# Optimization experiments

Measured on AMD Instinct MI355X. Metric: run time of the kernel, lower is better.

Reference implementation:

```python
import jax, jax.numpy as jnp
import numpy as np

NUM_VIRUSES = 50000
NUM_DRUGS = 50000
EMBED_DIM = 128
NUM_LAYERS = 3
NUM_INTERACTIONS = 800000  # undirected virus-drug pairs -> 1.6M directed edges


def setup_inputs() -> dict:
    key = jax.random.key(0)
    k1, k2, k3, k4 = jax.random.split(key, 4)
    n_nodes = NUM_VIRUSES + NUM_DRUGS
    # random bipartite interactions (virus -> global drug index)
    v = jax.random.randint(k1, (NUM_INTERACTIONS,), 0, NUM_VIRUSES)
    d = jax.random.randint(k2, (NUM_INTERACTIONS,), 0, NUM_DRUGS) + NUM_VIRUSES
    # symmetric adjacency: both directions
    edge_row = jnp.concatenate([v, d]).astype(jnp.int32)
    edge_col = jnp.concatenate([d, v]).astype(jnp.int32)
    # symmetric normalization D^{-1/2} A D^{-1/2}
    deg = jnp.zeros((n_nodes,), jnp.float32).at[edge_row].add(1.0)
    dinv_sqrt = jnp.where(deg > 0, jax.lax.rsqrt(jnp.maximum(deg, 1.0)), 0.0)
    edge_val = dinv_sqrt[edge_row] * dinv_sqrt[edge_col]
    virus_emb = jax.random.normal(k3, (NUM_VIRUSES, EMBED_DIM), dtype=jnp.float32) * 0.1
    drug_emb = jax.random.normal(k4, (NUM_DRUGS, EMBED_DIM), dtype=jnp.float32) * 0.1
    return {
        "edge_row": edge_row,
        "edge_col": edge_col,
        "edge_val": edge_val,
        "virus_emb": virus_emb,
        "drug_emb": drug_emb,
    }


def reference(edge_row, edge_col, edge_val, virus_emb, drug_emb):
    num_viruses = virus_emb.shape[0]
    n_nodes = num_viruses + drug_emb.shape[0]
    # initial layer-0 embeddings
    x = jnp.concatenate([virus_emb, drug_emb], axis=0)  # [N, D]
    acc = x  # running sum over layers (fused mean)
    h = x
    for _ in range(NUM_LAYERS):
        # SpMM: h <- A_norm @ h  via gather + segment_sum over COO edges
        msgs = edge_val[:, None] * h[edge_col]            # [nnz, D]
        h = jax.ops.segment_sum(msgs, edge_row, num_segments=n_nodes)
        acc = acc + h
    final = acc / jnp.asarray(NUM_LAYERS + 1, acc.dtype)  # mean over L+1 layers
    return final[:num_viruses, :], final[num_viruses:, :]
```

## Files before the change

### kernel.cpp

```cpp
#include <hip/hip_runtime.h>
#include <hip/hip_fp16.h>

static constexpr int D = 128;
static constexpr int RPB_LOG = 10;
static constexpr int RPB = 1 << RPB_LOG;
static constexpr int MAX_BINS = 1024;
static constexpr int CHUNK = 8192;

__global__ void binCount(const int* __restrict__ erow, int* __restrict__ bin_cnt,
                         int E, int nbins) {
    __shared__ int hist[MAX_BINS];
    int t = threadIdx.x;
    int e0 = blockIdx.x * CHUNK;
    for (int i = t; i < nbins; i += 256) hist[i] = 0;
    __syncthreads();
    for (int k = 0; k < CHUNK / 256; ++k) {
        int e = e0 + t + k * 256;
        if (e < E) atomicAdd(&hist[erow[e] >> RPB_LOG], 1);
    }
    __syncthreads();
    for (int b = t; b < nbins; b += 256)
        if (hist[b]) atomicAdd(&bin_cnt[b], hist[b]);
}

__global__ void scanBins(const int* __restrict__ bin_cnt, int* __restrict__ bin_base,
                         int* __restrict__ gcur, int nbins, int E) {
    __shared__ int sm[MAX_BINS];
    int t = threadIdx.x;
    int v = (t < nbins) ? bin_cnt[t] : 0;
    sm[t] = v;
    __syncthreads();
    for (int off = 1; off < MAX_BINS; off <<= 1) {
        int x = sm[t];
        int y = (t >= off) ? sm[t - off] : 0;
        __syncthreads();
        sm[t] = x + y;
        __syncthreads();
    }
    if (t < nbins) {
        int excl = sm[t] - v;
        bin_base[t] = excl;
        gcur[t] = excl;
    }
    if (t == 0) bin_base[nbins] = E;
}

__global__ void binA(const int* __restrict__ erow, const int* __restrict__ ecol,
                     int* __restrict__ gcur, int2* __restrict__ tmp, int E, int nbins) {
    __shared__ int hist[MAX_BINS];
    __shared__ int base[MAX_BINS];
    __shared__ int lcur[MAX_BINS];
    int t = threadIdx.x;
    int e0 = blockIdx.x * CHUNK;
    for (int i = t; i < nbins; i += 256) { hist[i] = 0; lcur[i] = 0; }
    __syncthreads();
    for (int k = 0; k < CHUNK / 256; ++k) {
        int e = e0 + t + k * 256;
        if (e < E) atomicAdd(&hist[erow[e] >> RPB_LOG], 1);
    }
    __syncthreads();
    for (int b = t; b < nbins; b += 256)
        base[b] = hist[b] ? atomicAdd(&gcur[b], hist[b]) : 0;
    __syncthreads();
    for (int k = 0; k < CHUNK / 256; ++k) {
        int e = e0 + t + k * 256;
        if (e < E) {
            int r = erow[e];
            int b = r >> RPB_LOG;
            int pos = base[b] + atomicAdd(&lcur[b], 1);
            tmp[pos] = make_int2(r, ecol[e]);
        }
    }
}

__global__ void binB(const int2* __restrict__ tmp, const int* __restrict__ bin_base,
                     int* __restrict__ row_ptr, float* __restrict__ dinv,
                     float* __restrict__ rdinv, int* __restrict__ col_s,
                     int N, int E, int nbins) {
    __shared__ int cnt[RPB];
    __shared__ int sm[RPB];
    __shared__ int cur[RPB];
    int b = blockIdx.x;
    int r0 = b << RPB_LOG;
    int t = threadIdx.x;
    cnt[t] = 0;
    __syncthreads();
    int start = bin_base[b];
    int end = bin_base[b + 1];
    for (int p = start + t; p < end; p += RPB)
        atomicAdd(&cnt[tmp[p].x - r0], 1);
    __syncthreads();
    int v = cnt[t];
    sm[t] = v;
    __syncthreads();
    for (int off = 1; off < RPB; off <<= 1) {
        int x = sm[t];
        int y = (t >= off) ? sm[t - off] : 0;
        __syncthreads();
        sm[t] = x + y;
        __syncthreads();
    }
    int rp = start + sm[t] - v;
    int r = r0 + t;
    if (r < N) {
        row_ptr[r] = rp;
        dinv[r]  = (v > 0) ? rsqrtf((float)v) : 0.0f;
        rdinv[r] = (v > 0) ? sqrtf((float)v) : 0.0f;
    }
    if (b == 0 && t == 0) row_ptr[N] = E;
    cur[t] = rp;
    __syncthreads();
    for (int p = start + t; p < end; p += RPB) {
        int2 pr = tmp[p];
        int pos = atomicAdd(&cur[pr.x - r0], 1);
        col_s[pos] = pr.y;
    }
}

__global__ void init_g(const float4* __restrict__ vsrc,
                       const float4* __restrict__ dsrc,
                       const float* __restrict__ dinv,
                       __half2* __restrict__ g,
                       long nv4, long total4) {
    long i = (long)blockIdx.x * blockDim.x + threadIdx.x;
    long stride = (long)gridDim.x * blockDim.x;
    for (; i < total4; i += stride) {
        float4 v = (i < nv4) ? vsrc[i] : dsrc[i - nv4];
        float w = dinv[i >> 5];
        g[i * 2]     = __floats2half2_rn(w * v.x, w * v.y);
        g[i * 2 + 1] = __floats2half2_rn(w * v.z, w * v.w);
    }
}

__device__ __forceinline__ void gather_rows(const int* __restrict__ col_s,
                                            int start, int end,
                                            const __half* __restrict__ gsrc,
                                            int grp, int sub, float acc[8]) {
    int j = start + grp;
    for (; j + 4 < end; j += 8) {
        int c0 = col_s[j];
        int c1 = col_s[j + 4];
        float4 v0 = ((const float4*)(gsrc + (long)c0 * D))[sub];
        float4 v1 = ((const float4*)(gsrc + (long)c1 * D))[sub];
        const __half2* h0 = (const __half2*)&v0;
        const __half2* h1 = (const __half2*)&v1;
#pragma unroll
        for (int k = 0; k < 4; ++k) {
            float2 f0 = __half22float2(h0[k]);
            float2 f1 = __half22float2(h1[k]);
            acc[2 * k]     += f0.x + f1.x;
            acc[2 * k + 1] += f0.y + f1.y;
        }
    }
    if (j < end) {
        int c = col_s[j];
        float4 v = ((const float4*)(gsrc + (long)c * D))[sub];
        const __half2* h = (const __half2*)&v;
#pragma unroll
        for (int k = 0; k < 4; ++k) {
            float2 f = __half22float2(h[k]);
            acc[2 * k]     += f.x;
            acc[2 * k + 1] += f.y;
        }
    }
#pragma unroll
    for (int k = 0; k < 8; ++k) {
        acc[k] += __shfl_xor(acc[k], 16, 64);
        acc[k] += __shfl_xor(acc[k], 32, 64);
    }
}

__global__ void spmm_mid(const int* __restrict__ row_ptr, const int* __restrict__ col_s,
                         const float* __restrict__ dinv, const __half* __restrict__ g,
                         __half* __restrict__ gnext, int N) {
    int gid = blockIdx.x * blockDim.x + threadIdx.x;
    int r = __builtin_amdgcn_readfirstlane(gid >> 6);
    if (r >= N) return;
    int lane = gid & 63;
    int grp = lane >> 4, sub = lane & 15;
    int start = row_ptr[r], end = row_ptr[r + 1];
    float acc[8] = {0, 0, 0, 0, 0, 0, 0, 0};
    gather_rows(col_s, start, end, g, grp, sub, acc);
    if (lane < 16) {
        float dr = dinv[r];
        float d2 = dr * dr;
        float4 st;
        __half2* hs = (__half2*)&st;
#pragma unroll
        for (int k = 0; k < 4; ++k)
            hs[k] = __floats2half2_rn(d2 * acc[2 * k], d2 * acc[2 * k + 1]);
        ((float4*)(gnext + (long)r * D))[sub] = st;
    }
}

__global__ void spmm_final(const int* __restrict__ row_ptr, const int* __restrict__ col_s,
                           const float* __restrict__ dinv, const float* __restrict__ rdinv,
                           const __half* __restrict__ g2,
                           const __half* __restrict__ g1,
                           const float* __restrict__ xv, const float* __restrict__ xd,
                           int nvRows, float* __restrict__ out, int N) {
    int gid = blockIdx.x * blockDim.x + threadIdx.x;
    int r = __builtin_amdgcn_readfirstlane(gid >> 6);
    if (r >= N) return;
    int lane = gid & 63;
    int grp = lane >> 4, sub = lane & 15;
    int start = row_ptr[r], end = row_ptr[r + 1];
    float acc[8] = {0, 0, 0, 0, 0, 0, 0, 0};
    gather_rows(col_s, start, end, g2, grp, sub, acc);
    if (lane < 16) {
        float dr = dinv[r];
        float rd = rdinv[r];
        const float* xbase = (r < nvRows) ? (xv + (long)r * D)
                                          : (xd + (long)(r - nvRows) * D);
        float4 x0 = ((const float4*)xbase)[sub * 2];
        float4 x1 = ((const float4*)xbase)[sub * 2 + 1];
        float4 p1v = ((const float4*)(g1 + (long)r * D))[sub];
        float4 p2v = ((const float4*)(g2 + (long)r * D))[sub];
        const __half2* h1 = (const __half2*)&p1v;
        const __half2* h2 = (const __half2*)&p2v;
        float xr[8] = {x0.x, x0.y, x0.z, x0.w, x1.x, x1.y, x1.z, x1.w};
        float o[8];
#pragma unroll
        for (int k = 0; k < 4; ++k) {
            float2 f1 = __half22float2(h1[k]);
            float2 f2 = __half22float2(h2[k]);
            o[2 * k]     = 0.25f * (xr[2 * k]     + (f1.x + f2.x) * rd + dr * acc[2 * k]);
            o[2 * k + 1] = 0.25f * (xr[2 * k + 1] + (f1.y + f2.y) * rd + dr * acc[2 * k + 1]);
        }
        float4* ob = (float4*)(out + (long)r * D);
        ob[sub * 2]     = make_float4(o[0], o[1], o[2], o[3]);
        ob[sub * 2 + 1] = make_float4(o[4], o[5], o[6], o[7]);
    }
}

__global__ void init_copy(const float4* __restrict__ vsrc,
                          const float4* __restrict__ dsrc,
                          float4* __restrict__ h,
                          float4* __restrict__ acc,
                          long nv4, long total4) {
    long i = (long)blockIdx.x * blockDim.x + threadIdx.x;
    long stride = (long)gridDim.x * blockDim.x;
    for (; i < total4; i += stride) {
        float4 v = (i < nv4) ? vsrc[i] : dsrc[i - nv4];
        h[i] = v;
        acc[i] = v;
    }
}

__global__ void spmm_scatter(const int* __restrict__ erow, const int* __restrict__ ecol,
                             const float* __restrict__ eval, const float* __restrict__ h,
                             float* __restrict__ hnext, int E) {
    long tid = (long)blockIdx.x * blockDim.x + threadIdx.x;
    int e = (int)(tid >> 6);
    if (e >= E) return;
    int lane = (int)(tid & 63);
    int r = erow[e], c = ecol[e];
    float w = eval[e];
    const float2* src = reinterpret_cast<const float2*>(h + (long)c * D);
    float2 m = src[lane];
    float* dst = hnext + (long)r * D + lane * 2;
    atomicAdd(dst, w * m.x);
    atomicAdd(dst + 1, w * m.y);
}

__global__ void add_scale(float4* __restrict__ acc, const float4* __restrict__ b,
                          float s, long total4) {
    long i = (long)blockIdx.x * blockDim.x + threadIdx.x;
    long stride = (long)gridDim.x * blockDim.x;
    for (; i < total4; i += stride) {
        float4 a = acc[i];
        float4 v = b[i];
        a.x = (a.x + v.x) * s;
        a.y = (a.y + v.y) * s;
        a.z = (a.z + v.z) * s;
        a.w = (a.w + v.w) * s;
        acc[i] = a;
    }
}

extern "C" void kernel_launch(void* const* d_in, const int* in_sizes, int n_in,
                              void* d_out, int out_size, void* d_ws, size_t ws_size,
                              hipStream_t stream) {
    const int*   erow = (const int*)d_in[0];
    const int*   ecol = (const int*)d_in[1];
    const float* eval = (const float*)d_in[2];
    const float* vemb = (const float*)d_in[3];
    const float* demb = (const float*)d_in[4];

    int  E   = in_sizes[0];
    long nvD = in_sizes[3];
    long ndD = in_sizes[4];
    long ND  = nvD + ndD;
    int  N   = (int)(ND / D);
    int  nvRows = (int)(nvD / D);
    int  nbins = (N + RPB - 1) >> RPB_LOG;

    float* out = (float*)d_out;

    char* w = (char*)d_ws;
    __half* gA = (__half*)w;  w += (size_t)ND * sizeof(__half);
    __half* gB = (__half*)w;  w += (size_t)ND * sizeof(__half);
    __half* gC = (__half*)w;  w += (size_t)ND * sizeof(__half);
    int* col_s    = (int*)w;  w += (size_t)E * sizeof(int);
    int2* tmp     = (int2*)w; w += (size_t)E * sizeof(int2);
    int* row_ptr  = (int*)w;  w += (size_t)(N + 1) * sizeof(int);
    int* bin_cnt  = (int*)w;  w += MAX_BINS * sizeof(int);
    int* bin_base = (int*)w;  w += (MAX_BINS + 1) * sizeof(int);
    int* gcur     = (int*)w;  w += MAX_BINS * sizeof(int);
    float* dinv   = (float*)w; w += (size_t)N * sizeof(float);
    float* rdinv  = (float*)w; w += (size_t)N * sizeof(float);
    size_t needed = (size_t)(w - (char*)d_ws);

    long total4 = ND / 4;
    long nv4    = nvD / 4;
    const int blk = 256;
    const int copyGrid = 2048;

    if (needed <= ws_size && nbins <= MAX_BINS) {
        hipMemsetAsync(bin_cnt, 0, MAX_BINS * sizeof(int), stream);
        int nblkA = (E + CHUNK - 1) / CHUNK;
        hipLaunchKernelGGL(binCount, dim3(nblkA), dim3(256), 0, stream,
                           erow, bin_cnt, E, nbins);
        hipLaunchKernelGGL(scanBins, dim3(1), dim3(1024), 0, stream,
                           bin_cnt, bin_base, gcur, nbins, E);
        hipLaunchKernelGGL(binA, dim3(nblkA), dim3(256), 0, stream,
                           erow, ecol, gcur, tmp, E, nbins);
        hipLaunchKernelGGL(binB, dim3(nbins), dim3(RPB), 0, stream,
                           tmp, bin_base, row_ptr, dinv, rdinv, col_s, N, E, nbins);

        hipLaunchKernelGGL(init_g, dim3(copyGrid), dim3(blk), 0, stream,
                           (const float4*)vemb, (const float4*)demb, dinv,
                           (__half2*)gA, nv4, total4);

        int rgrid = (int)(((long)N * 64 + blk - 1) / blk);
        hipLaunchKernelGGL(spmm_mid, dim3(rgrid), dim3(blk), 0, stream,
                           row_ptr, col_s, dinv, gA, gB, N);
        hipLaunchKernelGGL(spmm_mid, dim3(rgrid), dim3(blk), 0, stream,
                           row_ptr, col_s, dinv, gB, gC, N);
        hipLaunchKernelGGL(spmm_final, dim3(rgrid), dim3(blk), 0, stream,
                           row_ptr, col_s, dinv, rdinv, gC, gB,
                           vemb, demb, nvRows, out, N);
    } else {
        float* bufA = (float*)d_ws;
        float* bufB = bufA + ND;
        hipLaunchKernelGGL(init_copy, dim3(copyGrid), dim3(blk), 0, stream,
                           (const float4*)vemb, (const float4*)demb,
                           (float4*)bufA, (float4*)out, nv4, total4);
        float* cur = bufA;
        float* nxt = bufB;
        for (int l = 0; l < 3; ++l) {
            hipMemsetAsync(nxt, 0, (size_t)ND * sizeof(float), stream);
            long threads = (long)E * 64;
            int  sgrid   = (int)((threads + blk - 1) / blk);
            hipLaunchKernelGGL(spmm_scatter, dim3(sgrid), dim3(blk), 0, stream,
                               erow, ecol, eval, cur, nxt, E);
            float s = (l == 2) ? 0.25f : 1.0f;
            hipLaunchKernelGGL(add_scale, dim3(copyGrid), dim3(blk), 0, stream,
                               (float4*)out, (const float4*)nxt, s, total4);
            float* t = cur; cur = nxt; nxt = t;
        }
    }
}
```

Baseline: 266.0 us.

## Pack binned edges into one int, fuse init_g into binB, use wave-shuffle scans

Packs each binned edge's local row and column into a single 32-bit word instead of an int2, halving the temporary buffer traffic. The half-precision scaled initial embedding is now built inside binB, which removes the separate init_g launch and its extra read of dinv. The shared-memory Hillis-Steele scans are replaced with wave-shuffle scans, binning blocks are doubled in size, and the final output is written with nontemporal stores. The packing limits N to 2^20, which a new guard enforces, and binB's fused tail loop runs over only about 98 blocks, so the embedding conversion has limited parallelism.

```diff
diff --git a/kernel.cpp b/kernel.cpp
--- a/kernel.cpp
+++ b/kernel.cpp
@@ -5,40 +5,61 @@
 static constexpr int RPB_LOG = 10;
 static constexpr int RPB = 1 << RPB_LOG;
 static constexpr int MAX_BINS = 1024;
-static constexpr int CHUNK = 8192;
+static constexpr int CHUNK = 16384;
+
+typedef float f32x4 __attribute__((ext_vector_type(4)));
+__device__ __forceinline__ void nt_store4(float* p, float a, float b, float c, float d) {
+    f32x4 v = {a, b, c, d};
+    __builtin_nontemporal_store(v, (f32x4*)p);
+}
+
+__device__ __forceinline__ int excl_scan_1024(int v, int* wsum, int t) {
+    int x = v;
+#pragma unroll
+    for (int off = 1; off < 64; off <<= 1) {
+        int y = __shfl_up(x, off, 64);
+        if ((t & 63) >= off) x += y;
+    }
+    int wid = t >> 6;
+    if ((t & 63) == 63) wsum[wid] = x;
+    __syncthreads();
+    if (t < 16) {
+        int w = wsum[t];
+#pragma unroll
+        for (int off = 1; off < 16; off <<= 1) {
+            int y = __shfl_up(w, off, 64);
+            if (t >= off) w += y;
+        }
+        wsum[t] = w;
+    }
+    __syncthreads();
+    int base = (wid > 0) ? wsum[wid - 1] : 0;
+    return base + x - v;
+}
 
 __global__ void binCount(const int* __restrict__ erow, int* __restrict__ bin_cnt,
                          int E, int nbins) {
     __shared__ int hist[MAX_BINS];
     int t = threadIdx.x;
     int e0 = blockIdx.x * CHUNK;
-    for (int i = t; i < nbins; i += 256) hist[i] = 0;
-    __syncthreads();
-    for (int k = 0; k < CHUNK / 256; ++k) {
-        int e = e0 + t + k * 256;
+    for (int i = t; i < nbins; i += 512) hist[i] = 0;
+    __syncthreads();
+    for (int k = 0; k < CHUNK / 512; ++k) {
+        int e = e0 + t + k * 512;
         if (e < E) atomicAdd(&hist[erow[e] >> RPB_LOG], 1);
     }
     __syncthreads();
-    for (int b = t; b < nbins; b += 256)
+    for (int b = t; b < nbins; b += 512)
         if (hist[b]) atomicAdd(&bin_cnt[b], hist[b]);
 }
 
 __global__ void scanBins(const int* __restrict__ bin_cnt, int* __restrict__ bin_base,
                          int* __restrict__ gcur, int nbins, int E) {
-    __shared__ int sm[MAX_BINS];
+    __shared__ int wsum[16];
     int t = threadIdx.x;
     int v = (t < nbins) ? bin_cnt[t] : 0;
-    sm[t] = v;
-    __syncthreads();
-    for (int off = 1; off < MAX_BINS; off <<= 1) {
-        int x = sm[t];
-        int y = (t >= off) ? sm[t - off] : 0;
-        __syncthreads();
-        sm[t] = x + y;
-        __syncthreads();
-    }
+    int excl = excl_scan_1024(v, wsum, t);
     if (t < nbins) {
-        int excl = sm[t] - v;
         bin_base[t] = excl;
         gcur[t] = excl;
     }
@@ -46,40 +67,43 @@
 }
 
 __global__ void binA(const int* __restrict__ erow, const int* __restrict__ ecol,
-                     int* __restrict__ gcur, int2* __restrict__ tmp, int E, int nbins) {
+                     int* __restrict__ gcur, int* __restrict__ tmp, int E, int nbins) {
     __shared__ int hist[MAX_BINS];
     __shared__ int base[MAX_BINS];
     __shared__ int lcur[MAX_BINS];
     int t = threadIdx.x;
     int e0 = blockIdx.x * CHUNK;
-    for (int i = t; i < nbins; i += 256) { hist[i] = 0; lcur[i] = 0; }
-    __syncthreads();
-    for (int k = 0; k < CHUNK / 256; ++k) {
-        int e = e0 + t + k * 256;
+    for (int i = t; i < nbins; i += 512) { hist[i] = 0; lcur[i] = 0; }
+    __syncthreads();
+    for (int k = 0; k < CHUNK / 512; ++k) {
+        int e = e0 + t + k * 512;
         if (e < E) atomicAdd(&hist[erow[e] >> RPB_LOG], 1);
     }
     __syncthreads();
-    for (int b = t; b < nbins; b += 256)
+    for (int b = t; b < nbins; b += 512)
         base[b] = hist[b] ? atomicAdd(&gcur[b], hist[b]) : 0;
     __syncthreads();
-    for (int k = 0; k < CHUNK / 256; ++k) {
-        int e = e0 + t + k * 256;
+    for (int k = 0; k < CHUNK / 512; ++k) {
+        int e = e0 + t + k * 512;
         if (e < E) {
             int r = erow[e];
             int b = r >> RPB_LOG;
             int pos = base[b] + atomicAdd(&lcur[b], 1);
-            tmp[pos] = make_int2(r, ecol[e]);
-        }
-    }
-}
-
-__global__ void binB(const int2* __restrict__ tmp, const int* __restrict__ bin_base,
+            tmp[pos] = ((r & (RPB - 1)) << 20) | ecol[e];
+        }
+    }
+}
+
+__global__ void binB(const int* __restrict__ tmp, const int* __restrict__ bin_base,
                      int* __restrict__ row_ptr, float* __restrict__ dinv,
                      float* __restrict__ rdinv, int* __restrict__ col_s,
+                     const float4* __restrict__ xv, const float4* __restrict__ xd,
+                     int nvRows, __half* __restrict__ g0,
                      int N, int E, int nbins) {
     __shared__ int cnt[RPB];
-    __shared__ int sm[RPB];
     __shared__ int cur[RPB];
+    __shared__ float dls[RPB];
+    __shared__ int wsum[16];
     int b = blockIdx.x;
     int r0 = b << RPB_LOG;
     int t = threadIdx.x;
@@ -88,47 +112,42 @@
     int start = bin_base[b];
     int end = bin_base[b + 1];
     for (int p = start + t; p < end; p += RPB)
-        atomicAdd(&cnt[tmp[p].x - r0], 1);
-    __syncthreads();
-    int v = cnt[t];
-    sm[t] = v;
-    __syncthreads();
-    for (int off = 1; off < RPB; off <<= 1) {
-        int x = sm[t];
-        int y = (t >= off) ? sm[t - off] : 0;
-        __syncthreads();
-        sm[t] = x + y;
-        __syncthreads();
-    }
-    int rp = start + sm[t] - v;
+        atomicAdd(&cnt[((unsigned)tmp[p]) >> 20], 1);
+    __syncthreads();
+    int deg = cnt[t];
+    int rp = start + excl_scan_1024(deg, wsum, t);
     int r = r0 + t;
+    float dv = (deg > 0) ? rsqrtf((float)deg) : 0.0f;
     if (r < N) {
         row_ptr[r] = rp;
-        dinv[r]  = (v > 0) ? rsqrtf((float)v) : 0.0f;
-        rdinv[r] = (v > 0) ? sqrtf((float)v) : 0.0f;
+        dinv[r] = dv;
+        rdinv[r] = (deg > 0) ? sqrtf((float)deg) : 0.0f;
     }
     if (b == 0 && t == 0) row_ptr[N] = E;
     cur[t] = rp;
+    dls[t] = dv;
     __syncthreads();
     for (int p = start + t; p < end; p += RPB) {
-        int2 pr = tmp[p];
-        int pos = atomicAdd(&cur[pr.x - r0], 1);
-        col_s[pos] = pr.y;
-    }
-}
-
-__global__ void init_g(const float4* __restrict__ vsrc,
-                       const float4* __restrict__ dsrc,
-                       const float* __restrict__ dinv,
-                       __half2* __restrict__ g,
-                       long nv4, long total4) {
-    long i = (long)blockIdx.x * blockDim.x + threadIdx.x;
-    long stride = (long)gridDim.x * blockDim.x;
-    for (; i < total4; i += stride) {
-        float4 v = (i < nv4) ? vsrc[i] : dsrc[i - nv4];
-        float w = dinv[i >> 5];
-        g[i * 2]     = __floats2half2_rn(w * v.x, w * v.y);
-        g[i * 2 + 1] = __floats2half2_rn(w * v.z, w * v.w);
+        unsigned v = (unsigned)tmp[p];
+        int pos = atomicAdd(&cur[v >> 20], 1);
+        col_s[pos] = (int)(v & 0xFFFFF);
+    }
+    for (int idx = t; idx < RPB * 16; idx += RPB) {
+        int rr = r0 + (idx >> 4);
+        if (rr >= N) break;
+        int q = idx & 15;
+        float w = dls[idx >> 4];
+        const float4* src = (rr < nvRows) ? (xv + (long)rr * 32)
+                                          : (xd + (long)(rr - nvRows) * 32);
+        float4 a = src[q * 2];
+        float4 c = src[q * 2 + 1];
+        float4 st;
+        __half2* hs = (__half2*)&st;
+        hs[0] = __floats2half2_rn(w * a.x, w * a.y);
+        hs[1] = __floats2half2_rn(w * a.z, w * a.w);
+        hs[2] = __floats2half2_rn(w * c.x, w * c.y);
+        hs[3] = __floats2half2_rn(w * c.z, w * c.w);
+        ((float4*)(g0 + (long)rr * D))[q] = st;
     }
 }
 
@@ -227,9 +246,9 @@
             o[2 * k]     = 0.25f * (xr[2 * k]     + (f1.x + f2.x) * rd + dr * acc[2 * k]);
             o[2 * k + 1] = 0.25f * (xr[2 * k + 1] + (f1.y + f2.y) * rd + dr * acc[2 * k + 1]);
         }
-        float4* ob = (float4*)(out + (long)r * D);
-        ob[sub * 2]     = make_float4(o[0], o[1], o[2], o[3]);
-        ob[sub * 2 + 1] = make_float4(o[4], o[5], o[6], o[7]);
+        float* ob = out + (long)r * D + sub * 8;
+        nt_store4(ob,     o[0], o[1], o[2], o[3]);
+        nt_store4(ob + 4, o[4], o[5], o[6], o[7]);
     }
 }
 
@@ -302,7 +321,7 @@
     __half* gB = (__half*)w;  w += (size_t)ND * sizeof(__half);
     __half* gC = (__half*)w;  w += (size_t)ND * sizeof(__half);
     int* col_s    = (int*)w;  w += (size_t)E * sizeof(int);
-    int2* tmp     = (int2*)w; w += (size_t)E * sizeof(int2);
+    int* tmp      = (int*)w;  w += (size_t)E * sizeof(int);
     int* row_ptr  = (int*)w;  w += (size_t)(N + 1) * sizeof(int);
     int* bin_cnt  = (int*)w;  w += MAX_BINS * sizeof(int);
     int* bin_base = (int*)w;  w += (MAX_BINS + 1) * sizeof(int);
@@ -316,21 +335,19 @@
     const int blk = 256;
     const int copyGrid = 2048;
 
-    if (needed <= ws_size && nbins <= MAX_BINS) {
-        hipMemsetAsync(bin_cnt, 0, MAX_BINS * sizeof(int), stream);
+    if (needed <= ws_size && nbins <= MAX_BINS && N <= (1 << 20)) {
+        hipMemsetAsync(bin_cnt, 0, (size_t)nbins * sizeof(int), stream);
         int nblkA = (E + CHUNK - 1) / CHUNK;
-        hipLaunchKernelGGL(binCount, dim3(nblkA), dim3(256), 0, stream,
+        hipLaunchKernelGGL(binCount, dim3(nblkA), dim3(512), 0, stream,
                            erow, bin_cnt, E, nbins);
         hipLaunchKernelGGL(scanBins, dim3(1), dim3(1024), 0, stream,
                            bin_cnt, bin_base, gcur, nbins, E);
-        hipLaunchKernelGGL(binA, dim3(nblkA), dim3(256), 0, stream,
+        hipLaunchKernelGGL(binA, dim3(nblkA), dim3(512), 0, stream,
                            erow, ecol, gcur, tmp, E, nbins);
         hipLaunchKernelGGL(binB, dim3(nbins), dim3(RPB), 0, stream,
-                           tmp, bin_base, row_ptr, dinv, rdinv, col_s, N, E, nbins);
-
-        hipLaunchKernelGGL(init_g, dim3(copyGrid), dim3(blk), 0, stream,
-                           (const float4*)vemb, (const float4*)demb, dinv,
-                           (__half2*)gA, nv4, total4);
+                           tmp, bin_base, row_ptr, dinv, rdinv, col_s,
+                           (const float4*)vemb, (const float4*)demb,
+                           nvRows, gA, N, E, nbins);
 
         int rgrid = (int)(((long)N * 64 + blk - 1) / blk);
         hipLaunchKernelGGL(spmm_mid, dim3(rgrid), dim3(blk), 0, stream,
```

After: 255.7 us, median of 2. -3.9%, faster.
